# Kernel tuning notes

Hardware: AMD Instinct MI355X
Metric: run time of the kernel (lower is better)

The kernel has to match this reference:

```python
import jax, jax.numpy as jnp
import numpy as np

N_NODES = 100000
N_EDGES = 1600000
IN_FEAT = 128
HEADS = 4
OUT_FEAT = 16
ALPHA = 0.2  # LeakyReLU negative slope


def setup_inputs() -> dict:
    key = jax.random.key(0)
    k1, k2, k3, k4, k5 = jax.random.split(key, 5)
    x = jax.random.normal(k1, (N_NODES, IN_FEAT), dtype=jnp.float32)
    edge_index = jax.random.randint(k2, (2, N_EDGES), 0, N_NODES, dtype=jnp.int64)
    # xavier_uniform with gain=1.414
    gain = 1.414
    lim_W = gain * np.sqrt(6.0 / (IN_FEAT + HEADS * OUT_FEAT))
    W = jax.random.uniform(k3, (IN_FEAT, HEADS * OUT_FEAT), minval=-lim_W, maxval=lim_W, dtype=jnp.float32)
    lim_a = gain * np.sqrt(6.0 / (HEADS + OUT_FEAT))
    a_src = jax.random.uniform(k4, (HEADS, OUT_FEAT), minval=-lim_a, maxval=lim_a, dtype=jnp.float32)
    a_dst = jax.random.uniform(k5, (HEADS, OUT_FEAT), minval=-lim_a, maxval=lim_a, dtype=jnp.float32)
    return {"x": x, "edge_index": edge_index, "W": W, "a_src": a_src, "a_dst": a_dst}


def reference(x, edge_index, W, a_src, a_dst):
    N = x.shape[0]
    H, F = a_src.shape
    src, dst = edge_index[0], edge_index[1]

    h = (x @ W).reshape(N, H, F)                 # [N, H, F]
    att_src = jnp.sum(h * a_src, axis=-1)        # [N, H]
    att_dst = jnp.sum(h * a_dst, axis=-1)        # [N, H]

    e = jax.nn.leaky_relu(att_src[src] + att_dst[dst], negative_slope=ALPHA)  # [E, H]

    # segment softmax over edges grouped by dst
    e_max = jax.ops.segment_max(e, dst, num_segments=N)   # [N, H]
    e_max = jnp.where(jnp.isfinite(e_max), e_max, 0.0)    # nodes with no in-edges
    ex = jnp.exp(e - e_max[dst])                           # [E, H]
    denom = jax.ops.segment_sum(ex, dst, num_segments=N)  # [N, H]
    alpha = ex / (denom[dst] + 1e-16)                      # [E, H]
    # dropout: inference mode (training=False) -> identity

    messages = h[src] * alpha[:, :, None]                  # [E, H, F]
    out = jax.ops.segment_sum(messages, dst, num_segments=N)  # [N, H, F]

    out = out.reshape(N, H * F)  # concat=True
    out = jax.nn.elu(out)
    return out
```

## Files before the change

kernel.cpp:

```cpp
#include <hip/hip_runtime.h>


#define NEG_SLOPE 0.2f
#define BSHIFT 9
#define BNODES 512
#define CH 2048
#define BCB 512
#define CAP 24576

typedef __bf16 bf16x8 __attribute__((ext_vector_type(8)));
typedef float  f32x4  __attribute__((ext_vector_type(4)));

static __device__ __forceinline__ unsigned f2b(float f) {
    union { float f; unsigned u; } v; v.f = f;
    return (v.u + 0x7fffu + ((v.u >> 16) & 1u)) >> 16;
}
static __device__ __forceinline__ float u2f(unsigned u) {
    union { unsigned u32; float f; } v; v.u32 = u; return v.f;
}

__global__ __launch_bounds__(256) void gemm_att_kernel(
    const float* __restrict__ x,
    const float* __restrict__ W,
    const float* __restrict__ a_src,
    const float* __restrict__ a_dst,
    unsigned short* __restrict__ h_out,
    float* __restrict__ att_s_o,
    float* __restrict__ att_d_o,
    const int* __restrict__ dst,
    int* __restrict__ bucketCount,
    int N, int E, int gemmBlocks)
{
    __shared__ bf16x8 Wswz[20][64];
    __shared__ int c[256];
    int t = threadIdx.x;

    if (blockIdx.x >= gemmBlocks) {
        int bid = blockIdx.x - gemmBlocks;
        c[t] = 0;
        __syncthreads();
        for (int e = bid * 256 + t; e < E; e += BCB * 256)
            atomicAdd(&c[dst[e] >> BSHIFT], 1);
        __syncthreads();
        if (c[t]) atomicAdd(&bucketCount[t], c[t]);
        return;
    }

    for (int i = t; i < 8192; i += 256) {
        int k = i >> 6, n = i & 63;
        __bf16* dp = (__bf16*)&Wswz[((n >> 4) << 2) | (k >> 5)]
                                   [(((k >> 3) & 3) << 4) | (n & 15)];
        dp[k & 7] = (__bf16)W[i];
    }
    for (int i = t; i < 1024; i += 256) {
        int k = i >> 3, c7 = i & 7;
        int hd = c7 & 3;
        const float* aa = (c7 < 4) ? a_src : a_dst;
        float sum = 0.f;
        #pragma unroll
        for (int f = 0; f < 16; ++f)
            sum = fmaf(W[k * 64 + hd * 16 + f], aa[hd * 16 + f], sum);
        __bf16* dp = (__bf16*)&Wswz[16 + (k >> 5)][(((k >> 3) & 3) << 4) | c7];
        dp[k & 7] = (__bf16)sum;
        __bf16* dz = (__bf16*)&Wswz[16 + (k >> 5)][(((k >> 3) & 3) << 4) | (8 + c7)];
        dz[k & 7] = (__bf16)0.f;
    }
    __syncthreads();

    int wave = t >> 6;
    int lane = t & 63;
    int col = lane & 15, quad = lane >> 4;
    int node_base = (blockIdx.x * 4 + wave) * 16;
    int arow = min(node_base + col, N - 1);
    const float* xp = x + arow * 128;

    bf16x8 af[4];
    #pragma unroll
    for (int tt = 0; tt < 4; ++tt) {
        float4 xa = *(const float4*)(xp + tt * 32 + quad * 8);
        float4 xb = *(const float4*)(xp + tt * 32 + quad * 8 + 4);
        bf16x8 f;
        f[0] = (__bf16)xa.x; f[1] = (__bf16)xa.y;
        f[2] = (__bf16)xa.z; f[3] = (__bf16)xa.w;
        f[4] = (__bf16)xb.x; f[5] = (__bf16)xb.y;
        f[6] = (__bf16)xb.z; f[7] = (__bf16)xb.w;
        af[tt] = f;
    }

    f32x4 acc[4], accA;
    #pragma unroll
    for (int cb = 0; cb < 4; ++cb) {
        acc[cb] = (f32x4){0.f, 0.f, 0.f, 0.f};
        #pragma unroll
        for (int tt = 0; tt < 4; ++tt)
            acc[cb] = __builtin_amdgcn_mfma_f32_16x16x32_bf16(
                af[tt], Wswz[(cb << 2) | tt][lane], acc[cb], 0, 0, 0);
    }
    accA = (f32x4){0.f, 0.f, 0.f, 0.f};
    #pragma unroll
    for (int tt = 0; tt < 4; ++tt)
        accA = __builtin_amdgcn_mfma_f32_16x16x32_bf16(
            af[tt], Wswz[16 + tt][lane], accA, 0, 0, 0);

    #pragma unroll
    for (int cb = 0; cb < 4; ++cb) {
        #pragma unroll
        for (int r = 0; r < 4; ++r) {
            int node = node_base + quad * 4 + r;
            if (node < N)
                h_out[node * 64 + cb * 16 + col] = (unsigned short)f2b(acc[cb][r]);
        }
    }
    if (col < 8) {
        #pragma unroll
        for (int r = 0; r < 4; ++r) {
            int node = node_base + quad * 4 + r;
            if (node < N) {
                if (col < 4) att_s_o[(node << 2) | col] = accA[r];
                else         att_d_o[(node << 2) | (col - 4)] = accA[r];
            }
        }
    }
}

__global__ __launch_bounds__(256) void bscatter_kernel(
    const int* __restrict__ src, const int* __restrict__ dst,
    const int* __restrict__ bucketCount,
    int* __restrict__ bucketCursor, int* __restrict__ pairs, int nb, int E)
{
    __shared__ int cnt[256], lo[256], gpos[256], cur[256], sm[256], gbc[256];
    __shared__ int2 staged[CH];
    int t = threadIdx.x;
    int base = blockIdx.x * CH;
    int nloc = min(CH, E - base);

    cnt[t] = 0;
    gbc[t] = (t < nb) ? bucketCount[t] : 0;
    __syncthreads();
    for (int i = t; i < nloc; i += 256)
        atomicAdd(&cnt[dst[base + i] >> BSHIFT], 1);
    __syncthreads();

    int v = cnt[t];
    sm[t] = v;
    __syncthreads();
    #pragma unroll
    for (int off = 1; off < 256; off <<= 1) {
        int u = (t >= off) ? sm[t - off] : 0;
        __syncthreads();
        sm[t] += u;
        __syncthreads();
    }
    lo[t] = sm[t] - v;
    cur[t] = lo[t];
    __syncthreads();

    int g = gbc[t];
    sm[t] = g;
    __syncthreads();
    #pragma unroll
    for (int off = 1; off < 256; off <<= 1) {
        int u = (t >= off) ? sm[t - off] : 0;
        __syncthreads();
        sm[t] += u;
        __syncthreads();
    }
    gpos[t] = (v > 0) ? (sm[t] - g) + atomicAdd(&bucketCursor[t], v) : 0;
    __syncthreads();

    for (int i = t; i < nloc; i += 256) {
        int d = dst[base + i];
        int s = src[base + i];
        int b = d >> BSHIFT;
        int k = atomicAdd(&cur[b], 1);
        staged[k] = make_int2((s << BSHIFT) | (d & (BNODES - 1)), b);
    }
    __syncthreads();

    for (int i = t; i < nloc; i += 256) {
        int2 p = staged[i];
        pairs[gpos[p.y] + (i - lo[p.y])] = p.x;
    }
}

__global__ __launch_bounds__(1024) void bucket_csr_agg_kernel(
    const int* __restrict__ pairs,
    const int* __restrict__ bucketCount,
    const float* __restrict__ att_s,
    const float* __restrict__ att_d,
    const unsigned short* __restrict__ hmat,
    float* __restrict__ out,
    int nb, int N)
{
    extern __shared__ int sorted[];
    __shared__ int rs[BNODES + 1];
    __shared__ int cur[BNODES];
    __shared__ int sm[BNODES];
    __shared__ int gbc[256], gsm[256];
    __shared__ float attd[BNODES * 4];

    int b = blockIdx.x, t = threadIdx.x;
    int node_lo = b << BSHIFT;
    int nn = min(BNODES, N - node_lo);

    if (t < 256) { int g = (t < nb) ? bucketCount[t] : 0; gbc[t] = g; gsm[t] = g; }
    if (t < BNODES) cur[t] = 0;
    __syncthreads();
    #pragma unroll
    for (int off = 1; off < 256; off <<= 1) {
        int u = (t >= off && t < 256) ? gsm[t - off] : 0;
        __syncthreads();
        if (t < 256) gsm[t] += u;
        __syncthreads();
    }
    int ebase = gsm[b] - gbc[b];
    int ecnt  = gbc[b];

    for (int i = t; i < (nn << 2); i += 1024)
        attd[i] = att_d[(node_lo << 2) + i];

    for (int i = t; i < ecnt; i += 1024)
        atomicAdd(&cur[pairs[ebase + i] & (BNODES - 1)], 1);
    __syncthreads();

    int v = (t < BNODES) ? cur[t] : 0;
    if (t < BNODES) sm[t] = v;
    __syncthreads();
    #pragma unroll
    for (int off = 1; off < BNODES; off <<= 1) {
        int u = (t >= off && t < BNODES) ? sm[t - off] : 0;
        __syncthreads();
        if (t < BNODES) sm[t] += u;
        __syncthreads();
    }
    if (t < BNODES) { int x = sm[t] - v; rs[t] = x; cur[t] = x; }
    if (t == 0) rs[BNODES] = ecnt;
    __syncthreads();

    for (int i = t; i < ecnt; i += 1024) {
        int p = pairs[ebase + i];
        int k = atomicAdd(&cur[p & (BNODES - 1)], 1);
        sorted[k] = p >> BSHIFT;
    }
    __syncthreads();

    int q = t & 7;
    int grp = (t >> 3) & 7;
    int wv = t >> 6;
    int h = q >> 1;

    for (int pass = 0; pass < 4; ++pass) {
        int node = (wv << 5) + (pass << 3) + grp;
        if (node >= nn) continue;
        int beg = rs[node];
        int deg = rs[node + 1] - beg;
        float ad = attd[(node << 2) | h];

        float a0 = 0.f, a1 = 0.f, a2 = 0.f, a3 = 0.f;
        float a4 = 0.f, a5 = 0.f, a6 = 0.f, a7 = 0.f, l = 0.f;
        for (int e = 0; e < deg; ++e) {
            int s = sorted[beg + e];
            float av = att_s[(s << 2) | h] + ad;
            av = fmaxf(av, NEG_SLOPE * av);
            float w = __expf(av);
            l += w;
            uint4 hp = *(const uint4*)(hmat + (s << 6) + (q << 3));
            a0 = fmaf(w, u2f(hp.x << 16), a0);
            a1 = fmaf(w, u2f(hp.x & 0xffff0000u), a1);
            a2 = fmaf(w, u2f(hp.y << 16), a2);
            a3 = fmaf(w, u2f(hp.y & 0xffff0000u), a3);
            a4 = fmaf(w, u2f(hp.z << 16), a4);
            a5 = fmaf(w, u2f(hp.z & 0xffff0000u), a5);
            a6 = fmaf(w, u2f(hp.w << 16), a6);
            a7 = fmaf(w, u2f(hp.w & 0xffff0000u), a7);
        }

        float rl = 1.0f / (l + 1e-16f);
        float4 v0, v1;
        v0.x = a0 * rl; v0.x = (v0.x > 0.f) ? v0.x : (__expf(v0.x) - 1.f);
        v0.y = a1 * rl; v0.y = (v0.y > 0.f) ? v0.y : (__expf(v0.y) - 1.f);
        v0.z = a2 * rl; v0.z = (v0.z > 0.f) ? v0.z : (__expf(v0.z) - 1.f);
        v0.w = a3 * rl; v0.w = (v0.w > 0.f) ? v0.w : (__expf(v0.w) - 1.f);
        v1.x = a4 * rl; v1.x = (v1.x > 0.f) ? v1.x : (__expf(v1.x) - 1.f);
        v1.y = a5 * rl; v1.y = (v1.y > 0.f) ? v1.y : (__expf(v1.y) - 1.f);
        v1.z = a6 * rl; v1.z = (v1.z > 0.f) ? v1.z : (__expf(v1.z) - 1.f);
        v1.w = a7 * rl; v1.w = (v1.w > 0.f) ? v1.w : (__expf(v1.w) - 1.f);
        float* op = out + ((size_t)(node_lo + node) << 6) + (q << 3);
        *(float4*)op = v0;
        *(float4*)(op + 4) = v1;
    }
}

extern "C" void kernel_launch(void* const* d_in, const int* in_sizes, int n_in,
                              void* d_out, int out_size, void* d_ws, size_t ws_size,
                              hipStream_t stream) {
    const float* x     = (const float*)d_in[0];
    const int*   ei    = (const int*)d_in[1];
    const float* W     = (const float*)d_in[2];
    const float* a_src = (const float*)d_in[3];
    const float* a_dst = (const float*)d_in[4];

    int N = in_sizes[0] / 128;
    int E = in_sizes[1] / 2;
    const int* src = ei;
    const int* dst = ei + E;
    int nb = (N + BNODES - 1) / BNODES;

    char* ws = (char*)d_ws;
    size_t off = 0;
    unsigned short* hmat = (unsigned short*)(ws + off); off += (size_t)N * 64 * 2;
    float* att_s = (float*)(ws + off);  off += (size_t)N * 4 * 4;
    float* att_d = (float*)(ws + off);  off += (size_t)N * 4 * 4;
    int* pairs    = (int*)(ws + off);   off += (size_t)E * 4;
    int* bucketCount  = (int*)(ws + off); off += 256 * 4;
    int* bucketCursor = (int*)(ws + off); off += 256 * 4;

    hipMemsetAsync(bucketCount, 0, 512 * 4, stream);

    hipFuncSetAttribute((const void*)bucket_csr_agg_kernel,
                        hipFuncAttributeMaxDynamicSharedMemorySize,
                        CAP * 4);

    int gemmBlocks = (N + 63) / 64;
    gemm_att_kernel<<<gemmBlocks + BCB, 256, 0, stream>>>(
        x, W, a_src, a_dst, hmat, att_s, att_d, dst, bucketCount,
        N, E, gemmBlocks);

    int blocksS = (E + CH - 1) / CH;
    bscatter_kernel<<<blocksS, 256, 0, stream>>>(src, dst, bucketCount,
                                                 bucketCursor, pairs, nb, E);

    bucket_csr_agg_kernel<<<nb, 1024, CAP * 4, stream>>>(
        pairs, bucketCount, att_s, att_d, hmat, (float*)d_out, nb, N);
}
```

Baseline: 198.5 us.

## Split aggregation buckets into quarter blocks and unroll edge loop by four

The aggregation kernel now launches four 256-thread blocks per 512-node bucket. Each block filters the bucket's edges down to its own 128-node quarter and builds a small local CSR in static shared memory, so occupancy rises and the large dynamic shared buffer is no longer needed. The per-node edge loop is unrolled by four so several gathers of att_s and hmat are in flight at once. In exchange, every quarter block rereads the whole bucket's pair list twice. Edges beyond the fixed QCAP capacity are silently dropped while rs still counts them, so a heavy quarter would read past the sorted buffer.

```diff
diff --git a/kernel.cpp b/kernel.cpp
--- a/kernel.cpp
+++ b/kernel.cpp
@@ -6,7 +6,9 @@
 #define BNODES 512
 #define CH 2048
 #define BCB 512
-#define CAP 24576
+#define QSHIFT 7
+#define QNODES 128
+#define QCAP 2816
 
 typedef __bf16 bf16x8 __attribute__((ext_vector_type(8)));
 typedef float  f32x4  __attribute__((ext_vector_type(4)));
@@ -183,7 +185,7 @@
     }
 }
 
-__global__ __launch_bounds__(1024) void bucket_csr_agg_kernel(
+__global__ __launch_bounds__(256, 8) void bucket_csr_agg_kernel(
     const int* __restrict__ pairs,
     const int* __restrict__ bucketCount,
     const float* __restrict__ att_s,
@@ -192,65 +194,71 @@
     float* __restrict__ out,
     int nb, int N)
 {
-    extern __shared__ int sorted[];
-    __shared__ int rs[BNODES + 1];
-    __shared__ int cur[BNODES];
-    __shared__ int sm[BNODES];
+    __shared__ int sorted[QCAP];
+    __shared__ int cnt[QNODES], rs[QNODES + 1], cur[QNODES], sm[QNODES];
     __shared__ int gbc[256], gsm[256];
-    __shared__ float attd[BNODES * 4];
-
-    int b = blockIdx.x, t = threadIdx.x;
-    int node_lo = b << BSHIFT;
-    int nn = min(BNODES, N - node_lo);
-
-    if (t < 256) { int g = (t < nb) ? bucketCount[t] : 0; gbc[t] = g; gsm[t] = g; }
-    if (t < BNODES) cur[t] = 0;
+    __shared__ float attd[QNODES * 4];
+
+    int blk = blockIdx.x, t = threadIdx.x;
+    int b = blk >> 2, quar = blk & 3;
+    int node_lo = (b << BSHIFT) + (quar << QSHIFT);
+    if (node_lo >= N) return;
+    int nn = min(QNODES, N - node_lo);
+
+    { int g = (t < nb) ? bucketCount[t] : 0; gbc[t] = g; gsm[t] = g; }
+    if (t < QNODES) cnt[t] = 0;
     __syncthreads();
     #pragma unroll
     for (int off = 1; off < 256; off <<= 1) {
-        int u = (t >= off && t < 256) ? gsm[t - off] : 0;
-        __syncthreads();
-        if (t < 256) gsm[t] += u;
+        int u = (t >= off) ? gsm[t - off] : 0;
+        __syncthreads();
+        gsm[t] += u;
         __syncthreads();
     }
     int ebase = gsm[b] - gbc[b];
     int ecnt  = gbc[b];
 
-    for (int i = t; i < (nn << 2); i += 1024)
+    for (int i = t; i < (nn << 2); i += 256)
         attd[i] = att_d[(node_lo << 2) + i];
 
-    for (int i = t; i < ecnt; i += 1024)
-        atomicAdd(&cur[pairs[ebase + i] & (BNODES - 1)], 1);
-    __syncthreads();
-
-    int v = (t < BNODES) ? cur[t] : 0;
-    if (t < BNODES) sm[t] = v;
-    __syncthreads();
-    #pragma unroll
-    for (int off = 1; off < BNODES; off <<= 1) {
-        int u = (t >= off && t < BNODES) ? sm[t - off] : 0;
-        __syncthreads();
-        if (t < BNODES) sm[t] += u;
-        __syncthreads();
-    }
-    if (t < BNODES) { int x = sm[t] - v; rs[t] = x; cur[t] = x; }
-    if (t == 0) rs[BNODES] = ecnt;
-    __syncthreads();
-
-    for (int i = t; i < ecnt; i += 1024) {
+    for (int i = t; i < ecnt; i += 256) {
+        int dl = pairs[ebase + i] & (BNODES - 1);
+        if ((dl >> QSHIFT) == quar)
+            atomicAdd(&cnt[dl & (QNODES - 1)], 1);
+    }
+    __syncthreads();
+
+    int v = (t < QNODES) ? cnt[t] : 0;
+    if (t < QNODES) sm[t] = v;
+    __syncthreads();
+    #pragma unroll
+    for (int off = 1; off < QNODES; off <<= 1) {
+        int u = (t >= off && t < QNODES) ? sm[t - off] : 0;
+        __syncthreads();
+        if (t < QNODES) sm[t] += u;
+        __syncthreads();
+    }
+    if (t < QNODES) { int x = sm[t] - v; rs[t] = x; cur[t] = x; }
+    if (t == 0) rs[QNODES] = 0;
+    __syncthreads();
+    if (t == 0) rs[QNODES] = (QNODES <= nn) ? sm[QNODES - 1] : sm[QNODES - 1];
+    __syncthreads();
+
+    for (int i = t; i < ecnt; i += 256) {
         int p = pairs[ebase + i];
-        int k = atomicAdd(&cur[p & (BNODES - 1)], 1);
-        sorted[k] = p >> BSHIFT;
+        int dl = p & (BNODES - 1);
+        if ((dl >> QSHIFT) == quar) {
+            int k = atomicAdd(&cur[dl & (QNODES - 1)], 1);
+            if (k < QCAP) sorted[k] = p >> BSHIFT;
+        }
     }
     __syncthreads();
 
     int q = t & 7;
-    int grp = (t >> 3) & 7;
-    int wv = t >> 6;
     int h = q >> 1;
 
     for (int pass = 0; pass < 4; ++pass) {
-        int node = (wv << 5) + (pass << 3) + grp;
+        int node = (pass << 5) + (t >> 3);
         if (node >= nn) continue;
         int beg = rs[node];
         int deg = rs[node + 1] - beg;
@@ -258,21 +266,61 @@
 
         float a0 = 0.f, a1 = 0.f, a2 = 0.f, a3 = 0.f;
         float a4 = 0.f, a5 = 0.f, a6 = 0.f, a7 = 0.f, l = 0.f;
-        for (int e = 0; e < deg; ++e) {
-            int s = sorted[beg + e];
-            float av = att_s[(s << 2) | h] + ad;
-            av = fmaxf(av, NEG_SLOPE * av);
-            float w = __expf(av);
-            l += w;
-            uint4 hp = *(const uint4*)(hmat + (s << 6) + (q << 3));
-            a0 = fmaf(w, u2f(hp.x << 16), a0);
-            a1 = fmaf(w, u2f(hp.x & 0xffff0000u), a1);
-            a2 = fmaf(w, u2f(hp.y << 16), a2);
-            a3 = fmaf(w, u2f(hp.y & 0xffff0000u), a3);
-            a4 = fmaf(w, u2f(hp.z << 16), a4);
-            a5 = fmaf(w, u2f(hp.z & 0xffff0000u), a5);
-            a6 = fmaf(w, u2f(hp.w << 16), a6);
-            a7 = fmaf(w, u2f(hp.w & 0xffff0000u), a7);
+        int d1 = deg - 1;
+        for (int e0 = 0; e0 < deg; e0 += 4) {
+            int s0 = sorted[beg + min(e0 + 0, d1)];
+            int s1 = sorted[beg + min(e0 + 1, d1)];
+            int s2 = sorted[beg + min(e0 + 2, d1)];
+            int s3 = sorted[beg + min(e0 + 3, d1)];
+            float t0 = att_s[(s0 << 2) | h];
+            float t1 = att_s[(s1 << 2) | h];
+            float t2 = att_s[(s2 << 2) | h];
+            float t3 = att_s[(s3 << 2) | h];
+            uint4 hp0 = *(const uint4*)(hmat + (s0 << 6) + (q << 3));
+            uint4 hp1 = *(const uint4*)(hmat + (s1 << 6) + (q << 3));
+            uint4 hp2 = *(const uint4*)(hmat + (s2 << 6) + (q << 3));
+            uint4 hp3 = *(const uint4*)(hmat + (s3 << 6) + (q << 3));
+            float av0 = t0 + ad; av0 = fmaxf(av0, NEG_SLOPE * av0);
+            float av1 = t1 + ad; av1 = fmaxf(av1, NEG_SLOPE * av1);
+            float av2 = t2 + ad; av2 = fmaxf(av2, NEG_SLOPE * av2);
+            float av3 = t3 + ad; av3 = fmaxf(av3, NEG_SLOPE * av3);
+            float w0 = __expf(av0);
+            float w1 = (e0 + 1 < deg) ? __expf(av1) : 0.f;
+            float w2 = (e0 + 2 < deg) ? __expf(av2) : 0.f;
+            float w3 = (e0 + 3 < deg) ? __expf(av3) : 0.f;
+            l += w0 + w1 + w2 + w3;
+            a0 = fmaf(w0, u2f(hp0.x << 16), a0);
+            a1 = fmaf(w0, u2f(hp0.x & 0xffff0000u), a1);
+            a2 = fmaf(w0, u2f(hp0.y << 16), a2);
+            a3 = fmaf(w0, u2f(hp0.y & 0xffff0000u), a3);
+            a4 = fmaf(w0, u2f(hp0.z << 16), a4);
+            a5 = fmaf(w0, u2f(hp0.z & 0xffff0000u), a5);
+            a6 = fmaf(w0, u2f(hp0.w << 16), a6);
+            a7 = fmaf(w0, u2f(hp0.w & 0xffff0000u), a7);
+            a0 = fmaf(w1, u2f(hp1.x << 16), a0);
+            a1 = fmaf(w1, u2f(hp1.x & 0xffff0000u), a1);
+            a2 = fmaf(w1, u2f(hp1.y << 16), a2);
+            a3 = fmaf(w1, u2f(hp1.y & 0xffff0000u), a3);
+            a4 = fmaf(w1, u2f(hp1.z << 16), a4);
+            a5 = fmaf(w1, u2f(hp1.z & 0xffff0000u), a5);
+            a6 = fmaf(w1, u2f(hp1.w << 16), a6);
+            a7 = fmaf(w1, u2f(hp1.w & 0xffff0000u), a7);
+            a0 = fmaf(w2, u2f(hp2.x << 16), a0);
+            a1 = fmaf(w2, u2f(hp2.x & 0xffff0000u), a1);
+            a2 = fmaf(w2, u2f(hp2.y << 16), a2);
+            a3 = fmaf(w2, u2f(hp2.y & 0xffff0000u), a3);
+            a4 = fmaf(w2, u2f(hp2.z << 16), a4);
+            a5 = fmaf(w2, u2f(hp2.z & 0xffff0000u), a5);
+            a6 = fmaf(w2, u2f(hp2.w << 16), a6);
+            a7 = fmaf(w2, u2f(hp2.w & 0xffff0000u), a7);
+            a0 = fmaf(w3, u2f(hp3.x << 16), a0);
+            a1 = fmaf(w3, u2f(hp3.x & 0xffff0000u), a1);
+            a2 = fmaf(w3, u2f(hp3.y << 16), a2);
+            a3 = fmaf(w3, u2f(hp3.y & 0xffff0000u), a3);
+            a4 = fmaf(w3, u2f(hp3.z << 16), a4);
+            a5 = fmaf(w3, u2f(hp3.z & 0xffff0000u), a5);
+            a6 = fmaf(w3, u2f(hp3.w << 16), a6);
+            a7 = fmaf(w3, u2f(hp3.w & 0xffff0000u), a7);
         }
 
         float rl = 1.0f / (l + 1e-16f);
@@ -317,10 +365,6 @@
 
     hipMemsetAsync(bucketCount, 0, 512 * 4, stream);
 
-    hipFuncSetAttribute((const void*)bucket_csr_agg_kernel,
-                        hipFuncAttributeMaxDynamicSharedMemorySize,
-                        CAP * 4);
-
     int gemmBlocks = (N + 63) / 64;
     gemm_att_kernel<<<gemmBlocks + BCB, 256, 0, stream>>>(
         x, W, a_src, a_dst, hmat, att_s, att_d, dst, bucketCount,
@@ -330,6 +374,6 @@
     bscatter_kernel<<<blocksS, 256, 0, stream>>>(src, dst, bucketCount,
                                                  bucketCursor, pairs, nb, E);
 
-    bucket_csr_agg_kernel<<<nb, 1024, CAP * 4, stream>>>(
+    bucket_csr_agg_kernel<<<nb * 4, 256, 0, stream>>>(
         pairs, bucketCount, att_s, att_d, hmat, (float*)d_out, nb, N);
 }
```

New measurement: 211.3 us. +6.4%, slower.
